# Optimization experiments

Hardware: AMD Instinct MI355X
Metric: run time of the kernel (lower is better)

Reference implementation:

```python
import jax, jax.numpy as jnp
import numpy as np

D_MODEL = 1024
N_HEADS = 16
D_K = D_MODEL // N_HEADS


def setup_inputs() -> dict:
    key = jax.random.key(0)
    ks = jax.random.split(key, 5)
    x = jax.random.normal(ks[0], (4, 2048, D_MODEL), dtype=jnp.float32)
    # nn.Linear stores weight as [out, in]; we store transposed [in, out] for x @ W
    w_qkv = jax.random.normal(ks[1], (D_MODEL, 3 * D_MODEL), dtype=jnp.float32) / np.sqrt(D_MODEL)
    b_qkv = jnp.zeros((3 * D_MODEL,), dtype=jnp.float32)
    w_fc = jax.random.normal(ks[2], (D_MODEL, D_MODEL), dtype=jnp.float32) / np.sqrt(D_MODEL)
    b_fc = jnp.zeros((D_MODEL,), dtype=jnp.float32)
    ln_g = jnp.ones((D_MODEL,), dtype=jnp.float32)
    ln_b = jnp.zeros((D_MODEL,), dtype=jnp.float32)
    return {"x": x, "w_qkv": w_qkv, "b_qkv": b_qkv, "w_fc": w_fc, "b_fc": b_fc,
            "ln_g": ln_g, "ln_b": ln_b}


def _layernorm(x, g, b, eps=1e-5):
    mu = jnp.mean(x, axis=-1, keepdims=True)
    var = jnp.mean(jnp.square(x - mu), axis=-1, keepdims=True)
    return (x - mu) * jax.lax.rsqrt(var + eps) * g + b


def reference(x, w_qkv, b_qkv, w_fc, b_fc, ln_g, ln_b):
    residual = x
    xn = _layernorm(x, ln_g, ln_b)
    B, L, D = xn.shape
    qkv = xn @ w_qkv + b_qkv  # [B, L, 3D]
    q, k, v = jnp.split(qkv, 3, axis=-1)
    # b l (h d) -> b h l d
    def to_heads(t):
        return t.reshape(B, L, N_HEADS, D_K).transpose(0, 2, 1, 3)
    q, k, v = to_heads(q), to_heads(k), to_heads(v)
    scale = 1.0 / np.sqrt(D_K)
    scores = jnp.einsum('bhld,bhmd->bhlm', q, k) * scale  # [B,H,L,L]
    attn = jax.nn.softmax(scores, axis=-1)
    # dropout is identity in eval mode
    out = jnp.einsum('bhlm,bhmd->bhld', attn, v)  # [B,H,L,d]
    out = out.transpose(0, 2, 1, 3).reshape(B, L, D)  # b h l d -> b l (h d)
    out = out @ w_fc + b_fc
    return out + residual
```

## Files before the change

kernel.cpp:

```cpp
#include <hip/hip_runtime.h>
#include <hip/hip_bf16.h>
#include <cstdint>
#include <cstddef>

using bf16 = __hip_bfloat16;
typedef __attribute__((ext_vector_type(4))) float f32x4;
typedef __attribute__((ext_vector_type(8))) short bf16x8;

#define D_MODEL 1024
#define SEQ     2048
#define NB      4
#define NHEAD   16
#define DHEAD   64
#define NROWS   (NB * SEQ)

__device__ __forceinline__ void load_lds16(const void* g, void* l) {
  __builtin_amdgcn_global_load_lds(
      (const __attribute__((address_space(1))) unsigned int*)g,
      (__attribute__((address_space(3))) unsigned int*)l, 16, 0, 0);
}

__device__ __forceinline__ unsigned short f2bf(float f) {
  bf16 h = __float2bfloat16(f);
  return *(unsigned short*)&h;
}

__device__ __forceinline__ unsigned pk_trunc(float a, float b) {
  union { float f; unsigned u; } ca, cb;
  ca.f = a; cb.f = b;
  return (ca.u >> 16) | (cb.u & 0xffff0000u);
}

__global__ __launch_bounds__(256) void ln_kernel(
    const float* __restrict__ x, const float* __restrict__ g,
    const float* __restrict__ bb, bf16* __restrict__ xn) {
  int row  = blockIdx.x * 4 + (threadIdx.x >> 6);
  int lane = threadIdx.x & 63;
  const float4* xr = (const float4*)(x + (size_t)row * D_MODEL);
  float v[16], s = 0.f;
#pragma unroll
  for (int i = 0; i < 4; i++) {
    float4 t = xr[lane + 64 * i];
    v[4 * i] = t.x; v[4 * i + 1] = t.y; v[4 * i + 2] = t.z; v[4 * i + 3] = t.w;
    s += t.x + t.y + t.z + t.w;
  }
#pragma unroll
  for (int off = 32; off; off >>= 1) s += __shfl_xor(s, off, 64);
  float mean = s * (1.f / D_MODEL);
  float vs = 0.f;
#pragma unroll
  for (int i = 0; i < 16; i++) { float d = v[i] - mean; vs += d * d; }
#pragma unroll
  for (int off = 32; off; off >>= 1) vs += __shfl_xor(vs, off, 64);
  float rstd = rsqrtf(vs * (1.f / D_MODEL) + 1e-5f);
  ushort4* op = (ushort4*)(xn + (size_t)row * D_MODEL);
#pragma unroll
  for (int i = 0; i < 4; i++) {
    float4 gv = ((const float4*)g)[lane + 64 * i];
    float4 bv = ((const float4*)bb)[lane + 64 * i];
    ushort4 o;
    o.x = f2bf((v[4 * i]     - mean) * rstd * gv.x + bv.x);
    o.y = f2bf((v[4 * i + 1] - mean) * rstd * gv.y + bv.y);
    o.z = f2bf((v[4 * i + 2] - mean) * rstd * gv.z + bv.z);
    o.w = f2bf((v[4 * i + 3] - mean) * rstd * gv.w + bv.w);
    op[lane + 64 * i] = o;
  }
}

__global__ __launch_bounds__(256) void transpose_kernel(
    const float* __restrict__ in, bf16* __restrict__ out, int R, int C) {
  __shared__ float tile[32][33];
  int c0 = blockIdx.x * 32, r0 = blockIdx.y * 32;
  int tx = threadIdx.x & 31, ty = threadIdx.x >> 5;
  for (int i = ty; i < 32; i += 8)
    tile[i][tx] = in[(size_t)(r0 + i) * C + c0 + tx];
  __syncthreads();
  for (int i = ty; i < 32; i += 8)
    out[(size_t)(c0 + i) * R + r0 + tx] = __float2bfloat16(tile[tx][i]);
}

__device__ __forceinline__ void store_ct(bf16* p, float v)  { *p = __float2bfloat16(v); }
__device__ __forceinline__ void store_ct(float* p, float v) { *p = v; }

template <int SPLIT, int RESID, typename CT>
__global__ __launch_bounds__(256) void gemm_bt(
    const bf16* __restrict__ A, const bf16* __restrict__ Bt,
    const float* __restrict__ bias, const float* __restrict__ resid,
    CT* __restrict__ C, bf16* __restrict__ vt, int M, int N, int K) {
  __shared__ __attribute__((aligned(16))) bf16 Alds[128 * 32];
  __shared__ __attribute__((aligned(16))) bf16 Blds[128 * 32];
  int tid = threadIdx.x, wave = tid >> 6, lane = tid & 63;
  int ntiles = N >> 7;
  int bm = blockIdx.x / ntiles, bn = blockIdx.x % ntiles;
  int m0 = bm << 7, n0 = bn << 7;
  int wm = (wave >> 1) << 6, wn = (wave & 1) << 6;
  int srow = tid >> 2, scol = (tid & 3) * 8;
  int frow = lane & 15, fk = (lane >> 4) * 8;
  const bf16* Ap  = A  + (size_t)(m0 + srow) * K + scol;
  const bf16* Ap2 = A  + (size_t)(m0 + 64 + srow) * K + scol;
  const bf16* Bp  = Bt + (size_t)(n0 + srow) * K + scol;
  const bf16* Bp2 = Bt + (size_t)(n0 + 64 + srow) * K + scol;
  f32x4 acc[4][4] = {};
  for (int k0 = 0; k0 < K; k0 += 32) {
    __syncthreads();
    load_lds16(Ap,  (char*)Alds + tid * 16);
    load_lds16(Ap2, (char*)Alds + 4096 + tid * 16);
    load_lds16(Bp,  (char*)Blds + tid * 16);
    load_lds16(Bp2, (char*)Blds + 4096 + tid * 16);
    Ap += 32; Ap2 += 32; Bp += 32; Bp2 += 32;
    __syncthreads();
    bf16x8 af[4], bv[4];
#pragma unroll
    for (int i = 0; i < 4; i++)
      af[i] = *(const bf16x8*)&Alds[(wm + i * 16 + frow) * 32 + fk];
#pragma unroll
    for (int j = 0; j < 4; j++)
      bv[j] = *(const bf16x8*)&Blds[(wn + j * 16 + frow) * 32 + fk];
#pragma unroll
    for (int i = 0; i < 4; i++)
#pragma unroll
      for (int j = 0; j < 4; j++)
        acc[i][j] = __builtin_amdgcn_mfma_f32_16x16x32_bf16(af[i], bv[j], acc[i][j], 0, 0, 0);
  }
#pragma unroll
  for (int i = 0; i < 4; i++) {
    int row0 = m0 + wm + i * 16 + ((lane >> 4) << 2);
#pragma unroll
    for (int j = 0; j < 4; j++) {
      int col = n0 + wn + j * 16 + (lane & 15);
      float bvs = bias[col];
      if (SPLIT && col >= 2048) {
        int hd = col - 2048;
        int b = row0 >> 11, seq0 = row0 & 2047;
        int within = seq0 & 63, mt = within >> 4, q4 = (within >> 2) & 3;
        int pos = (seq0 & ~63) + ((mt >> 1) << 5) + (q4 << 3) + ((mt & 1) << 2);
        ushort4 pk;
        pk.x = f2bf(acc[i][j][0] + bvs);
        pk.y = f2bf(acc[i][j][1] + bvs);
        pk.z = f2bf(acc[i][j][2] + bvs);
        pk.w = f2bf(acc[i][j][3] + bvs);
        *(ushort4*)&vt[((size_t)(b * 1024 + hd)) * SEQ + pos] = pk;
      } else {
        int stride = SPLIT ? 2048 : N;
        float scale = (SPLIT && col < 1024) ? 0.18033688f : 1.0f;
#pragma unroll
        for (int r = 0; r < 4; r++) {
          size_t idx = (size_t)(row0 + r) * stride + col;
          float val = (acc[i][j][r] + bvs) * scale;
          if (RESID) val += resid[idx];
          store_ct(&C[idx], val);
        }
      }
    }
  }
}

__global__ __launch_bounds__(256, 4) void attn_kernel(
    const bf16* __restrict__ qk, const bf16* __restrict__ vt,
    bf16* __restrict__ aout) {
  int bh = blockIdx.x;
  int qt = blockIdx.y;
  int bb = bh >> 4, h = bh & 15;
  const bf16* Qg = qk + (size_t)bb * SEQ * 2048 + h * DHEAD;
  const bf16* Kg = Qg + D_MODEL;
  const bf16* Vg = vt + (size_t)bh * DHEAD * SEQ;

  __shared__ __attribute__((aligned(16))) bf16 Qlds[128 * 64];
  __shared__ __attribute__((aligned(16))) bf16 Klds[64 * 64];
  __shared__ __attribute__((aligned(16))) bf16 Vlds[64 * 64];

  int tid = threadIdx.x, wave = tid >> 6, lane = tid & 63;
  int prow = tid >> 3, pch = tid & 7;
  int lch8 = ((pch ^ (prow & 7)) << 3);
  int frow = lane & 15, quad = lane >> 4;
  int e0 = ((quad ^ (frow & 7)) << 3);
  int q0 = qt * 128;

#pragma unroll
  for (int s2 = 0; s2 < 4; s2++)
    load_lds16(Qg + (size_t)(q0 + s2 * 32 + prow) * 2048 + lch8,
               (char*)Qlds + s2 * 4096 + tid * 16);
  __syncthreads();
  bf16x8 qf[2][2];
#pragma unroll
  for (int qtile = 0; qtile < 2; qtile++)
#pragma unroll
    for (int kk = 0; kk < 2; kk++)
      qf[qtile][kk] =
          *(const bf16x8*)&Qlds[(wave * 32 + qtile * 16 + frow) * 64 + (e0 ^ (kk * 32))];

  f32x4 l4[2] = {};
  f32x4 o[4][2] = {};

  for (int kt = 0; kt < SEQ / 64; kt++) {
    int kv0 = kt * 64;
    __syncthreads();
#pragma unroll
    for (int s2 = 0; s2 < 2; s2++) {
      load_lds16(Kg + (size_t)(kv0 + s2 * 32 + prow) * 2048 + lch8,
                 (char*)Klds + s2 * 4096 + tid * 16);
      load_lds16(Vg + (size_t)(s2 * 32 + prow) * SEQ + kv0 + lch8,
                 (char*)Vlds + s2 * 4096 + tid * 16);
    }
    __syncthreads();

    f32x4 s[4][2] = {};
#pragma unroll
    for (int mt = 0; mt < 4; mt++) {
      bf16x8 af0 = *(const bf16x8*)&Klds[(mt * 16 + frow) * 64 + e0];
      bf16x8 af1 = *(const bf16x8*)&Klds[(mt * 16 + frow) * 64 + (e0 ^ 32)];
#pragma unroll
      for (int qtile = 0; qtile < 2; qtile++) {
        s[mt][qtile] = __builtin_amdgcn_mfma_f32_16x16x32_bf16(af0, qf[qtile][0], s[mt][qtile], 0, 0, 0);
        s[mt][qtile] = __builtin_amdgcn_mfma_f32_16x16x32_bf16(af1, qf[qtile][1], s[mt][qtile], 0, 0, 0);
      }
    }

    uint2 pk[2][4];
#pragma unroll
    for (int qtile = 0; qtile < 2; qtile++)
#pragma unroll
      for (int mt = 0; mt < 4; mt++) {
        f32x4 pv;
        pv[0] = __builtin_amdgcn_exp2f(s[mt][qtile][0]);
        pv[1] = __builtin_amdgcn_exp2f(s[mt][qtile][1]);
        pv[2] = __builtin_amdgcn_exp2f(s[mt][qtile][2]);
        pv[3] = __builtin_amdgcn_exp2f(s[mt][qtile][3]);
        l4[qtile] += pv;
        pk[qtile][mt].x = pk_trunc(pv[0], pv[1]);
        pk[qtile][mt].y = pk_trunc(pv[2], pv[3]);
      }

#pragma unroll
    for (int dt = 0; dt < 4; dt++) {
      bf16x8 vf0 = *(const bf16x8*)&Vlds[(dt * 16 + frow) * 64 + e0];
      bf16x8 vf1 = *(const bf16x8*)&Vlds[(dt * 16 + frow) * 64 + (e0 ^ 32)];
#pragma unroll
      for (int qtile = 0; qtile < 2; qtile++) {
        union { unsigned u[4]; bf16x8 v; } pf0, pf1;
        pf0.u[0] = pk[qtile][0].x; pf0.u[1] = pk[qtile][0].y;
        pf0.u[2] = pk[qtile][1].x; pf0.u[3] = pk[qtile][1].y;
        pf1.u[0] = pk[qtile][2].x; pf1.u[1] = pk[qtile][2].y;
        pf1.u[2] = pk[qtile][3].x; pf1.u[3] = pk[qtile][3].y;
        o[dt][qtile] = __builtin_amdgcn_mfma_f32_16x16x32_bf16(vf0, pf0.v, o[dt][qtile], 0, 0, 0);
        o[dt][qtile] = __builtin_amdgcn_mfma_f32_16x16x32_bf16(vf1, pf1.v, o[dt][qtile], 0, 0, 0);
      }
    }
  }

  float linv[2];
#pragma unroll
  for (int qtile = 0; qtile < 2; qtile++) {
    float v = (l4[qtile][0] + l4[qtile][1]) + (l4[qtile][2] + l4[qtile][3]);
    v += __shfl_xor(v, 16, 64);
    v += __shfl_xor(v, 32, 64);
    linv[qtile] = 1.f / v;
  }

  __syncthreads();
  bf16* Tw = (wave == 0) ? Qlds
           : (wave == 1) ? Qlds + 32 * 80
           : (wave == 2) ? Klds : Vlds;
#pragma unroll
  for (int qtile = 0; qtile < 2; qtile++)
#pragma unroll
    for (int dt = 0; dt < 4; dt++) {
      ushort4 pk;
      pk.x = f2bf(o[dt][qtile][0] * linv[qtile]);
      pk.y = f2bf(o[dt][qtile][1] * linv[qtile]);
      pk.z = f2bf(o[dt][qtile][2] * linv[qtile]);
      pk.w = f2bf(o[dt][qtile][3] * linv[qtile]);
      *(ushort4*)&Tw[(qtile * 16 + frow) * 80 + dt * 16 + quad * 4] = pk;
    }
  int rq = lane >> 1, d0 = (lane & 1) * 32;
  size_t grow = (size_t)(bb * SEQ + q0 + wave * 32 + rq);
#pragma unroll
  for (int i = 0; i < 4; i++) {
    bf16x8 v8 = *(const bf16x8*)&Tw[rq * 80 + d0 + i * 8];
    *(bf16x8*)&aout[grow * D_MODEL + h * DHEAD + d0 + i * 8] = v8;
  }
}

extern "C" void kernel_launch(void* const* d_in, const int* in_sizes, int n_in,
                              void* d_out, int out_size, void* d_ws, size_t ws_size,
                              hipStream_t stream) {
  const float* x     = (const float*)d_in[0];
  const float* w_qkv = (const float*)d_in[1];
  const float* b_qkv = (const float*)d_in[2];
  const float* w_fc  = (const float*)d_in[3];
  const float* b_fc  = (const float*)d_in[4];
  const float* ln_g  = (const float*)d_in[5];
  const float* ln_b  = (const float*)d_in[6];
  float* out = (float*)d_out;

  char* ws = (char*)d_ws;
  bf16* xn    = (bf16*)(ws);
  bf16* wqkvT = (bf16*)(ws + (16u << 20));
  bf16* wfcT  = (bf16*)(ws + (22u << 20));
  bf16* qk    = (bf16*)(ws + (24u << 20));
  bf16* vt    = (bf16*)(ws + (56u << 20));
  bf16* aout  = (bf16*)(ws);

  ln_kernel<<<NROWS / 4, 256, 0, stream>>>(x, ln_g, ln_b, xn);
  transpose_kernel<<<dim3(3 * D_MODEL / 32, D_MODEL / 32), 256, 0, stream>>>(
      w_qkv, wqkvT, D_MODEL, 3 * D_MODEL);
  transpose_kernel<<<dim3(D_MODEL / 32, D_MODEL / 32), 256, 0, stream>>>(
      w_fc, wfcT, D_MODEL, D_MODEL);
  gemm_bt<1, 0, bf16><<<(NROWS / 128) * (3 * D_MODEL / 128), 256, 0, stream>>>(
      xn, wqkvT, b_qkv, nullptr, qk, vt, NROWS, 3 * D_MODEL, D_MODEL);
  attn_kernel<<<dim3(NB * NHEAD, SEQ / 128), 256, 0, stream>>>(qk, vt, aout);
  gemm_bt<0, 1, float><<<(NROWS / 128) * (D_MODEL / 128), 256, 0, stream>>>(
      aout, wfcT, b_fc, x, out, nullptr, NROWS, D_MODEL, D_MODEL);
}
```

Before: 286.5 us.

## Double GEMM K-tile to 64 with XOR-swizzled LDS and merge weight transposes

The GEMM now stages a 64-wide K slice per iteration instead of 32. This halves the number of barrier pairs and doubles the MFMA work between them. LDS columns are XOR-swizzled by row to avoid bank conflicts on the wider rows. Separately, the two weight transpose launches are merged into one grid, which saves a kernel launch. LDS use per block doubles, which may lower occupancy.

```diff
diff --git a/kernel.cpp b/kernel.cpp
--- a/kernel.cpp
+++ b/kernel.cpp
@@ -68,15 +68,19 @@
 }
 
 __global__ __launch_bounds__(256) void transpose_kernel(
-    const float* __restrict__ in, bf16* __restrict__ out, int R, int C) {
+    const float* __restrict__ w_qkv, bf16* __restrict__ wqkvT,
+    const float* __restrict__ w_fc, bf16* __restrict__ wfcT) {
   __shared__ float tile[32][33];
-  int c0 = blockIdx.x * 32, r0 = blockIdx.y * 32;
+  const float* in; bf16* out; int C, c0;
+  if (blockIdx.x < 96) { in = w_qkv; out = wqkvT; C = 3072; c0 = blockIdx.x * 32; }
+  else                 { in = w_fc;  out = wfcT;  C = 1024; c0 = (blockIdx.x - 96) * 32; }
+  int r0 = blockIdx.y * 32;
   int tx = threadIdx.x & 31, ty = threadIdx.x >> 5;
   for (int i = ty; i < 32; i += 8)
     tile[i][tx] = in[(size_t)(r0 + i) * C + c0 + tx];
   __syncthreads();
   for (int i = ty; i < 32; i += 8)
-    out[(size_t)(c0 + i) * R + r0 + tx] = __float2bfloat16(tile[tx][i]);
+    out[(size_t)(c0 + i) * 1024 + r0 + tx] = __float2bfloat16(tile[tx][i]);
 }
 
 __device__ __forceinline__ void store_ct(bf16* p, float v)  { *p = __float2bfloat16(v); }
@@ -87,47 +91,56 @@
     const bf16* __restrict__ A, const bf16* __restrict__ Bt,
     const float* __restrict__ bias, const float* __restrict__ resid,
     CT* __restrict__ C, bf16* __restrict__ vt, int M, int N, int K) {
-  __shared__ __attribute__((aligned(16))) bf16 Alds[128 * 32];
-  __shared__ __attribute__((aligned(16))) bf16 Blds[128 * 32];
+  __shared__ __attribute__((aligned(16))) bf16 Alds[128 * 64];
+  __shared__ __attribute__((aligned(16))) bf16 Blds[128 * 64];
   int tid = threadIdx.x, wave = tid >> 6, lane = tid & 63;
   int ntiles = N >> 7;
   int bm = blockIdx.x / ntiles, bn = blockIdx.x % ntiles;
   int m0 = bm << 7, n0 = bn << 7;
   int wm = (wave >> 1) << 6, wn = (wave & 1) << 6;
-  int srow = tid >> 2, scol = (tid & 3) * 8;
-  int frow = lane & 15, fk = (lane >> 4) * 8;
-  const bf16* Ap  = A  + (size_t)(m0 + srow) * K + scol;
-  const bf16* Ap2 = A  + (size_t)(m0 + 64 + srow) * K + scol;
-  const bf16* Bp  = Bt + (size_t)(n0 + srow) * K + scol;
-  const bf16* Bp2 = Bt + (size_t)(n0 + 64 + srow) * K + scol;
+  int srow = tid >> 3;
+  int sw8  = (((tid & 7) ^ (srow & 7)) << 3);
+  int frow = lane & 15, quad = lane >> 4;
+  const bf16* Ap[4];
+  const bf16* Bp[4];
+#pragma unroll
+  for (int s = 0; s < 4; s++) {
+    Ap[s] = A  + (size_t)(m0 + s * 32 + srow) * K + sw8;
+    Bp[s] = Bt + (size_t)(n0 + s * 32 + srow) * K + sw8;
+  }
   f32x4 acc[4][4] = {};
-  for (int k0 = 0; k0 < K; k0 += 32) {
+  for (int k0 = 0; k0 < K; k0 += 64) {
     __syncthreads();
-    load_lds16(Ap,  (char*)Alds + tid * 16);
-    load_lds16(Ap2, (char*)Alds + 4096 + tid * 16);
-    load_lds16(Bp,  (char*)Blds + tid * 16);
-    load_lds16(Bp2, (char*)Blds + 4096 + tid * 16);
-    Ap += 32; Ap2 += 32; Bp += 32; Bp2 += 32;
+#pragma unroll
+    for (int s = 0; s < 4; s++) {
+      load_lds16(Ap[s], (char*)Alds + s * 4096 + tid * 16);
+      load_lds16(Bp[s], (char*)Blds + s * 4096 + tid * 16);
+      Ap[s] += 64; Bp[s] += 64;
+    }
     __syncthreads();
-    bf16x8 af[4], bv[4];
+    bf16x8 af[4][2], bv[4][2];
 #pragma unroll
     for (int i = 0; i < 4; i++)
-      af[i] = *(const bf16x8*)&Alds[(wm + i * 16 + frow) * 32 + fk];
-#pragma unroll
-    for (int j = 0; j < 4; j++)
-      bv[j] = *(const bf16x8*)&Blds[(wn + j * 16 + frow) * 32 + fk];
+#pragma unroll
+      for (int kk = 0; kk < 2; kk++) {
+        int e = (((kk * 4 + quad) ^ (frow & 7)) << 3);
+        af[i][kk] = *(const bf16x8*)&Alds[(wm + i * 16 + frow) * 64 + e];
+        bv[i][kk] = *(const bf16x8*)&Blds[(wn + i * 16 + frow) * 64 + e];
+      }
 #pragma unroll
     for (int i = 0; i < 4; i++)
 #pragma unroll
-      for (int j = 0; j < 4; j++)
-        acc[i][j] = __builtin_amdgcn_mfma_f32_16x16x32_bf16(af[i], bv[j], acc[i][j], 0, 0, 0);
+      for (int j = 0; j < 4; j++) {
+        acc[i][j] = __builtin_amdgcn_mfma_f32_16x16x32_bf16(af[i][0], bv[j][0], acc[i][j], 0, 0, 0);
+        acc[i][j] = __builtin_amdgcn_mfma_f32_16x16x32_bf16(af[i][1], bv[j][1], acc[i][j], 0, 0, 0);
+      }
   }
 #pragma unroll
   for (int i = 0; i < 4; i++) {
-    int row0 = m0 + wm + i * 16 + ((lane >> 4) << 2);
+    int row0 = m0 + wm + i * 16 + (quad << 2);
 #pragma unroll
     for (int j = 0; j < 4; j++) {
-      int col = n0 + wn + j * 16 + (lane & 15);
+      int col = n0 + wn + j * 16 + frow;
       float bvs = bias[col];
       if (SPLIT && col >= 2048) {
         int hd = col - 2048;
@@ -302,10 +315,7 @@
   bf16* aout  = (bf16*)(ws);
 
   ln_kernel<<<NROWS / 4, 256, 0, stream>>>(x, ln_g, ln_b, xn);
-  transpose_kernel<<<dim3(3 * D_MODEL / 32, D_MODEL / 32), 256, 0, stream>>>(
-      w_qkv, wqkvT, D_MODEL, 3 * D_MODEL);
-  transpose_kernel<<<dim3(D_MODEL / 32, D_MODEL / 32), 256, 0, stream>>>(
-      w_fc, wfcT, D_MODEL, D_MODEL);
+  transpose_kernel<<<dim3(128, 32), 256, 0, stream>>>(w_qkv, wqkvT, w_fc, wfcT);
   gemm_bt<1, 0, bf16><<<(NROWS / 128) * (3 * D_MODEL / 128), 256, 0, stream>>>(
       xn, wqkvT, b_qkv, nullptr, qk, vt, NROWS, 3 * D_MODEL, D_MODEL);
   attn_kernel<<<dim3(NB * NHEAD, SEQ / 128), 256, 0, stream>>>(qk, vt, aout);
```

New measurement: 273.6 us. -4.5%, faster.
